# Kernel optimization log

Hardware: AMD Instinct MI355X
Metric: run time of the kernel (lower is better)

Reference implementation:

```python
import jax, jax.numpy as jnp
import numpy as np

B, S, HID = 1, 2048, 2048
H, KVH, D = 32, 8, 64
NUM_MASKS = 3
ROPE_THETA = 10000.0


def rope_tables(seq_len, dim, theta=ROPE_THETA):
    inv_freq = 1.0 / (theta ** (np.arange(0, dim, 2, dtype=np.float32) / dim))
    t = np.arange(seq_len, dtype=np.float32)
    freqs = np.outer(t, inv_freq)                      # [S, D/2]
    emb = np.concatenate([freqs, freqs], axis=-1)      # [S, D]
    return jnp.asarray(np.cos(emb))[None], jnp.asarray(np.sin(emb))[None]  # [1,S,D]


def setup_inputs() -> dict:
    key = jax.random.key(0)
    ks = jax.random.split(key, 5)
    cos, sin = rope_tables(S, D)
    sc = 1.0 / np.sqrt(HID)
    return {
        "hidden_states": jax.random.normal(ks[0], (B, S, HID), jnp.float32),
        "cos": cos, "sin": sin,
        "Wq": jax.random.normal(ks[1], (HID, H * D), jnp.float32) * sc,
        "Wk": jax.random.normal(ks[2], (HID, KVH * D), jnp.float32) * sc,
        "Wv": jax.random.normal(ks[3], (HID, KVH * D), jnp.float32) * sc,
        "Wo": jax.random.normal(ks[4], (H * D, HID), jnp.float32) * sc,
        "num_masks": NUM_MASKS,
    }


def rotate_half(x):
    x1, x2 = jnp.split(x, 2, axis=-1)
    return jnp.concatenate([-x2, x1], axis=-1)


def block_causal_bias(seq_len, num_mask, dtype):
    block_size = num_mask + 1
    i = jnp.arange(seq_len)[:, None]
    j = jnp.arange(seq_len)[None, :]
    causal = j <= i
    column = causal & (j % (num_mask + 1) == 0)
    block = causal & ((i // block_size) == (j // block_size))
    allowed = column | block
    neg = jnp.asarray(jnp.finfo(dtype).min if dtype != jnp.float32 else -jnp.inf, dtype)
    return jnp.where(allowed, jnp.asarray(0.0, dtype), neg)  # [S,S]


def reference(hidden_states, cos, sin, Wq, Wk, Wv, Wo, num_masks):
    b, s, _ = hidden_states.shape
    scaling = D ** -0.5
    # projections -> [B, heads, S, D]
    q = (hidden_states @ Wq).reshape(b, s, H, D).transpose(0, 2, 1, 3)
    k = (hidden_states @ Wk).reshape(b, s, KVH, D).transpose(0, 2, 1, 3)
    v = (hidden_states @ Wv).reshape(b, s, KVH, D).transpose(0, 2, 1, 3)
    # RoPE (cos/sin: [1,S,D] -> [1,1,S,D])
    c, sn = cos[:, None], sin[:, None]
    q = q * c + rotate_half(q) * sn
    k = k * c + rotate_half(k) * sn
    # GQA: repeat kv heads
    g = H // KVH
    k = jnp.repeat(k, g, axis=1)
    v = jnp.repeat(v, g, axis=1)
    bias = block_causal_bias(s, num_masks, hidden_states.dtype)  # [S,S]
    scores = jnp.einsum("bhqd,bhkd->bhqk", q, k) * scaling + bias[None, None]
    probs = jax.nn.softmax(scores, axis=-1)
    out = jnp.einsum("bhqk,bhkd->bhqd", probs, v)  # [B,H,S,D]
    out = out.transpose(0, 2, 1, 3).reshape(b, s, H * D)
    return out @ Wo
```

## Files before the change

### kernel.cpp

```cpp
#include <hip/hip_runtime.h>
#include <hip/hip_bf16.h>
#include <stdint.h>

#define S_LEN  2048
#define HIDDEN 2048
#define NH     32
#define NKVH   8
#define HD     64
#define NHD    (NH*HD)
#define KVD    (NKVH*HD)

typedef __attribute__((ext_vector_type(8))) short  short8;
typedef __attribute__((ext_vector_type(4))) short  short4v;
typedef __attribute__((ext_vector_type(4))) float  f32x4;
typedef __attribute__((ext_vector_type(4))) float  float4v;
typedef __attribute__((ext_vector_type(8))) __bf16 bf16x8;

#define WAITVM8()  asm volatile("s_waitcnt vmcnt(8)" ::: "memory")
#define WAITVM4()  asm volatile("s_waitcnt vmcnt(4)" ::: "memory")
#define WAITVM0()  asm volatile("s_waitcnt vmcnt(0)" ::: "memory")
#define ABARRIER() asm volatile("s_barrier" ::: "memory")

__device__ __forceinline__ short f2bf(float x){
  uint32_t u = __builtin_bit_cast(uint32_t, x);
  u += 0x7fffu + ((u >> 16) & 1u);
  return (short)(u >> 16);
}

__device__ __forceinline__ f32x4 mfma_bf16(short8 a, short8 b, f32x4 c){
  return __builtin_amdgcn_mfma_f32_16x16x32_bf16(
      __builtin_bit_cast(bf16x8, a), __builtin_bit_cast(bf16x8, b), c, 0, 0, 0);
}

__device__ __forceinline__ void gload16(const short* g, short* l){
  __builtin_amdgcn_global_load_lds(
      (const __attribute__((address_space(1))) void*)g,
      (__attribute__((address_space(3))) void*)l, 16, 0, 0);
}

__global__ __launch_bounds__(256) void k_prep(const float* __restrict__ hs,
                                              short* __restrict__ hsb,
                                              const float* __restrict__ Wq, short* __restrict__ WqT,
                                              const float* __restrict__ Wk, short* __restrict__ WkT,
                                              const float* __restrict__ Wv, short* __restrict__ WvT){
  int bid = blockIdx.x;
  if (bid < 4096){
    int i = bid*256 + threadIdx.x;
    float4v v = ((const float4v* __restrict__)hs)[i];
    short4v o;
#pragma unroll
    for (int j=0;j<4;j++) o[j] = f2bf(v[j]);
    ((short4v* __restrict__)hsb)[i] = o;
    return;
  }
  bid -= 4096;
  const float* W; short* WT; int R, C, GX;
  if (bid < 4096)      { W = Wq; WT = WqT; R = HIDDEN; C = NHD; GX = 64; }
  else if (bid < 5120) { bid -= 4096; W = Wk; WT = WkT; R = HIDDEN; C = KVD; GX = 16; }
  else                 { bid -= 5120; W = Wv; WT = WvT; R = HIDDEN; C = KVD; GX = 16; }
  const int bx = bid % GX, by = bid / GX;
  __shared__ float tile[32][33];
  const int x = threadIdx.x & 31, y0 = threadIdx.x >> 5;
  const int c0 = bx*32, r0 = by*32;
#pragma unroll
  for (int yy=y0; yy<32; yy+=8) tile[yy][x] = W[(size_t)(r0+yy)*C + c0 + x];
  __syncthreads();
#pragma unroll
  for (int yy=y0; yy<32; yy+=8) WT[(size_t)(c0+yy)*R + r0 + x] = f2bf(tile[x][yy]);
}

struct GemmIdx {
  int wid, r, g, wr, wc, kg, gtid, srow, c8, sx;
};
__device__ __forceinline__ GemmIdx gemm_idx(){
  GemmIdx ix;
  int tid = threadIdx.x, lane = tid&63;
  ix.kg = tid>>8; ix.gtid = tid&255;
  ix.wid = (tid>>6)&3; ix.r = lane&15; ix.g = lane>>4;
  ix.wr = ix.wid>>1; ix.wc = ix.wid&1;
  const int gt = ix.gtid;
  const int row0 = ((gt>>2) ^ (gt>>4)) & 1;
  ix.srow = (((gt>>3)<<1) | row0);
  ix.c8   = ((gt ^ (gt>>2) ^ (gt>>4)) & 1) | ((((gt>>1) ^ (gt>>3)) & 1) << 1);
  ix.sx   = (ix.r & 7) << 3;
  return ix;
}

__device__ __forceinline__ void compute128(const short* As, const short* Bs,
                                           f32x4 acc[4][4], const GemmIdx& ix){
  short8 af[4], bf[4];
#pragma unroll
  for (int m=0;m<4;m++)
    af[m] = *(const short8*)&As[((ix.wr*64 + m*16 + ix.r)*32 + ix.g*8) ^ ix.sx];
#pragma unroll
  for (int n=0;n<4;n++)
    bf[n] = *(const short8*)&Bs[((ix.wc*64 + n*16 + ix.r)*32 + ix.g*8) ^ ix.sx];
#pragma unroll
  for (int m=0;m<4;m++)
#pragma unroll
    for (int n=0;n<4;n++) acc[m][n] = mfma_bf16(af[m], bf[n], acc[m][n]);
}

__device__ __forceinline__ void red_groups(short* LDS, f32x4 acc[4][4], const GemmIdx& ix){
  __syncthreads();
  float* red = (float*)LDS;
  if (ix.kg){
#pragma unroll
    for (int m=0;m<4;m++)
#pragma unroll
      for (int n=0;n<4;n++)
#pragma unroll
        for (int j=0;j<4;j++)
          red[ix.wid*4096 + (m*16 + ix.g*4 + j)*64 + n*16 + ix.r] = acc[m][n][j];
  }
  __syncthreads();
  if (!ix.kg){
#pragma unroll
    for (int m=0;m<4;m++)
#pragma unroll
      for (int n=0;n<4;n++)
#pragma unroll
        for (int j=0;j<4;j++)
          acc[m][n][j] += red[ix.wid*4096 + (m*16 + ix.g*4 + j)*64 + n*16 + ix.r];
  }
}

template<int NKT>
__device__ __forceinline__ void gemm_core2(const short* __restrict__ A,
                                           const short* __restrict__ BT,
                                           int bm, int bn, short* LDS,
                                           f32x4 acc[4][4], const GemmIdx& ix){
  const int K = HIDDEN;
  const short* gA = A  + (size_t)(bm*128 + ix.srow)*K + ix.kg*(NKT*32) + ix.c8*8;
  const short* gB = BT + (size_t)(bn*128 + ix.srow)*K + ix.kg*(NKT*32) + ix.c8*8;
  short* L = LDS + ix.kg*16384;
  const int w = ix.gtid>>6;

#pragma unroll
  for (int m=0;m<4;m++)
#pragma unroll
    for (int n=0;n<4;n++) acc[m][n] = (f32x4){0.f,0.f,0.f,0.f};

  auto STAGE = [&](int buf, int kt){
    short* As_ = L + buf*8192;
    gload16(gA + kt*32,                As_ + w*512);
    gload16(gA + (size_t)64*K + kt*32, As_ + 2048 + w*512);
    gload16(gB + kt*32,                As_ + 4096 + w*512);
    gload16(gB + (size_t)64*K + kt*32, As_ + 6144 + w*512);
  };

  STAGE(0, 0);
  __syncthreads();
  for (int u=0; u<NKT/2; ++u){
    const int t = 2*u;
    if (t+1 < NKT) STAGE(1, t+1);
    compute128(L, L + 4096, acc, ix);
    __syncthreads();
    if (t+2 < NKT) STAGE(0, t+2);
    compute128(L + 8192, L + 12288, acc, ix);
    __syncthreads();
  }
  red_groups(LDS, acc, ix);
}

template<int NKT>
__device__ __forceinline__ void gemm_core3(const short* __restrict__ A,
                                           const short* __restrict__ BT,
                                           int bm, int bn, short* LDS,
                                           f32x4 acc[4][4], const GemmIdx& ix){
  const int K = HIDDEN;
  const short* gA = A  + (size_t)(bm*128 + ix.srow)*K + ix.kg*(NKT*32) + ix.c8*8;
  const short* gB = BT + (size_t)(bn*128 + ix.srow)*K + ix.kg*(NKT*32) + ix.c8*8;
  short* L = LDS + ix.kg*24576;
  const int w = ix.gtid>>6;

#pragma unroll
  for (int m=0;m<4;m++)
#pragma unroll
    for (int n=0;n<4;n++) acc[m][n] = (f32x4){0.f,0.f,0.f,0.f};

  auto STAGE = [&](int buf, int kt){
    short* As_ = L + buf*8192;
    gload16(gA + kt*32,                As_ + w*512);
    gload16(gA + (size_t)64*K + kt*32, As_ + 2048 + w*512);
    gload16(gB + kt*32,                As_ + 4096 + w*512);
    gload16(gB + (size_t)64*K + kt*32, As_ + 6144 + w*512);
  };

  STAGE(0, 0);
  STAGE(1, 1);
  int cur = 0;
  for (int t=0; t<NKT-2; ++t){
    int nxt = cur+2; if (nxt>=3) nxt-=3;
    STAGE(nxt, t+2);
    WAITVM8();
    ABARRIER();
    compute128(L + cur*8192, L + cur*8192 + 4096, acc, ix);
    ABARRIER();
    cur = (cur==2) ? 0 : cur+1;
  }
  WAITVM4();
  ABARRIER();
  compute128(L + cur*8192, L + cur*8192 + 4096, acc, ix);
  ABARRIER();
  cur = (cur==2) ? 0 : cur+1;
  WAITVM0();
  ABARRIER();
  compute128(L + cur*8192, L + cur*8192 + 4096, acc, ix);

  red_groups(LDS, acc, ix);
}

__global__ __launch_bounds__(512, 4) void k_gemm_qkv(const short* __restrict__ hsb,
                                                     const short* __restrict__ WqT,
                                                     const short* __restrict__ WkT,
                                                     const short* __restrict__ WvT,
                                                     const float* __restrict__ cosT,
                                                     const float* __restrict__ sinT,
                                                     const int* __restrict__ nm,
                                                     const float* __restrict__ Wo,
                                                     short* __restrict__ WoT,
                                                     short* __restrict__ Qb,
                                                     short* __restrict__ Kb,
                                                     short* __restrict__ VT,
                                                     short* __restrict__ VTs){
  __shared__ short LDS[32768];
  const int bn = blockIdx.x, bm = blockIdx.y;
  GemmIdx ix = gemm_idx();
  f32x4 acc[4][4];

  if (bn < 16){
    gemm_core2<32>(hsb, WqT + (size_t)bn*128*HIDDEN, bm, 0, LDS, acc, ix);
    if (ix.kg) return;
    const int h2 = bn*2 + ix.wc;
#pragma unroll
    for (int m=0;m<4;m++)
#pragma unroll
      for (int j=0;j<4;j++){
        const int s = bm*128 + ix.wr*64 + m*16 + ix.g*4 + j;
        const float* cr = cosT + s*64;
        const float* sr = sinT + s*64;
#pragma unroll
        for (int n=0;n<2;n++){
          const int d = n*16 + ix.r;
          float x1 = acc[m][n][j], x2 = acc[m][n+2][j];
          Qb[(size_t)s*NHD + h2*64 + d]      = f2bf((x1*cr[d]    - x2*sr[d])   *0.125f);
          Qb[(size_t)s*NHD + h2*64 + d + 32] = f2bf((x2*cr[d+32] + x1*sr[d+32])*0.125f);
        }
      }
  } else if (bn < 20){
    gemm_core2<32>(hsb, WkT + (size_t)(bn-16)*128*HIDDEN, bm, 0, LDS, acc, ix);
    if (ix.kg) return;
    const int h2 = (bn-16)*2 + ix.wc;
#pragma unroll
    for (int m=0;m<4;m++)
#pragma unroll
      for (int j=0;j<4;j++){
        const int s = bm*128 + ix.wr*64 + m*16 + ix.g*4 + j;
        const float* cr = cosT + s*64;
        const float* sr = sinT + s*64;
#pragma unroll
        for (int n=0;n<2;n++){
          const int d = n*16 + ix.r;
          float x1 = acc[m][n][j], x2 = acc[m][n+2][j];
          Kb[(size_t)s*KVD + h2*64 + d]      = f2bf(x1*cr[d]    - x2*sr[d]);
          Kb[(size_t)s*KVD + h2*64 + d + 32] = f2bf(x2*cr[d+32] + x1*sr[d+32]);
        }
      }
  } else if (bn < 24){
    gemm_core2<32>(hsb, WvT + (size_t)(bn-20)*128*HIDDEN, bm, 0, LDS, acc, ix);
    const int bs  = nm[0] + 1;
    const int lbs = 31 - __clz(bs);
    const int d0  = (bn-20)*128;
    const int s0  = bm*128;
    short* Vt = LDS;
    __syncthreads();
    if (!ix.kg){
#pragma unroll
      for (int n=0;n<4;n++){
        const int dr = ix.wc*64 + n*16 + ix.r;
#pragma unroll
        for (int m=0;m<4;m++){
          const int sc_ = ix.wr*64 + m*16 + ix.g*4;
          short4v o;
#pragma unroll
          for (int j=0;j<4;j++) o[j] = f2bf(acc[m][n][j]);
          *(short4v*)&Vt[dr*136 + sc_] = o;
        }
      }
    }
    __syncthreads();
    const int tid = threadIdx.x;
#pragma unroll
    for (int it=0; it<4; ++it){
      const int row = tid>>2, c8 = (tid&3)*32 + it*8;
      *(short8*)&VT[(size_t)(d0+row)*S_LEN + s0 + c8] = *(short8*)&Vt[row*136 + c8];
    }
    const int cnt = 128 >> lbs;
    for (int e = tid; e < 128*cnt; e += 512){
      const int row = e >> (7 - lbs), c = e & (cnt - 1);
      VTs[(size_t)(d0+row)*S_LEN + (s0>>lbs) + c] = Vt[row*136 + (c<<lbs)];
    }
  } else {
    const int bnt = bn - 24;
    float* tf = (float*)LDS;
    const int tid = threadIdx.x;
    const int half = tid >> 8;
    const int x = tid & 31, y0 = (tid >> 5) & 7;
    const int c0base = bnt*512, r0base = bm*128;
    for (int it=0; it<32; ++it){
      const int t = it*2 + half;
      const int c0 = c0base + (t & 15)*32;
      const int r0 = r0base + (t >> 4)*32;
      __syncthreads();
#pragma unroll
      for (int yy=y0; yy<32; yy+=8)
        tf[half*1056 + yy*33 + x] = Wo[(size_t)(r0+yy)*HIDDEN + c0 + x];
      __syncthreads();
#pragma unroll
      for (int yy=y0; yy<32; yy+=8)
        WoT[(size_t)(c0+yy)*NHD + r0 + x] = f2bf(tf[half*1056 + x*33 + yy]);
    }
  }
}

__global__ __launch_bounds__(512, 4) void k_gemm(const short* __restrict__ A,
                                                 const short* __restrict__ BT,
                                                 float* __restrict__ C, int Nc){
  __shared__ short LDS[49152];
  const int bn = blockIdx.x, bm = blockIdx.y;
  GemmIdx ix = gemm_idx();
  f32x4 acc[4][4];
  gemm_core3<32>(A, BT, bm, bn, LDS, acc, ix);
  if (ix.kg) return;
#pragma unroll
  for (int m=0;m<4;m++)
#pragma unroll
    for (int n=0;n<4;n++)
#pragma unroll
      for (int j=0;j<4;j++)
        C[(size_t)(bm*128 + ix.wr*64 + m*16 + ix.g*4 + j)*Nc
          + bn*128 + ix.wc*64 + n*16 + ix.r] = acc[m][n][j];
}


#define BF16_ONE 16256

__device__ __forceinline__ void sm_pv1(f32x4 sc[4],
                                       f32x4& accl,
                                       f32x4 acc[4], short* Pw,
                                       const short* Vtile,
                                       int r, int g){
  const short8 ones = {BF16_ONE,BF16_ONE,BF16_ONE,BF16_ONE,
                       BF16_ONE,BF16_ONE,BF16_ONE,BF16_ONE};
#pragma unroll
  for (int n=0;n<4;n++)
#pragma unroll
    for (int j=0;j<4;j++)
      Pw[(g*4+j)*72 + n*16 + r] = f2bf(__expf(sc[n][j]));

  short8 pf0 = *(short8*)&Pw[r*72 + g*8];
  short8 pf1 = *(short8*)&Pw[r*72 + 32 + g*8];
  accl = mfma_bf16(pf0, ones, accl);
  accl = mfma_bf16(pf1, ones, accl);
#pragma unroll
  for (int f=0;f<4;f++){
    short8 vf0 = *(const short8*)(Vtile + (size_t)(f*16 + r)*S_LEN + g*8);
    short8 vf1 = *(const short8*)(Vtile + (size_t)(f*16 + r)*S_LEN + 32 + g*8);
    acc[f] = mfma_bf16(pf0, vf0, acc[f]);
    acc[f] = mfma_bf16(pf1, vf1, acc[f]);
  }
}

__global__ __launch_bounds__(64, 4) void k_attn3(const short* __restrict__ Qb,
                                                 const short* __restrict__ Kb,
                                                 const short* __restrict__ VT,
                                                 const short* __restrict__ VTs,
                                                 const int* __restrict__ nm,
                                                 short* __restrict__ Ob){
  const int i  = gridDim.x - 1 - blockIdx.x;
  const int qs = i >> 5;
  const int h  = i & 31;
  const int hk = h >> 2;
  const int bs = nm[0] + 1;

  const int lane = threadIdx.x;
  const int r = lane&15, g = lane>>4;

  __shared__ short Pw[16*72];

  const int qlo = qs*16;

  short8 qf0 = *(const short8*)(Qb + (size_t)(qlo + r)*NHD + h*HD + g*8);
  short8 qf1 = *(const short8*)(Qb + (size_t)(qlo + r)*NHD + h*HD + 32 + g*8);

  f32x4 acc[4];
  f32x4 accl = (f32x4){0.f,0.f,0.f,0.f};
#pragma unroll
  for (int f=0;f<4;f++) acc[f] = (f32x4){0.f,0.f,0.f,0.f};

  const short* Kg  = Kb  + hk*HD;
  const short* Vsg = VTs + (size_t)hk*HD*S_LEN;
  const short* Vdg = VT  + (size_t)hk*HD*S_LEN;

  const int cmax = qlo / bs;
  const int nct = (cmax + 63) >> 6;
  for (int ct=0; ct<nct; ++ct){
    const int cbase = ct*64;
    f32x4 sc[4];
#pragma unroll
    for (int n=0;n<4;n++){
      const int key = bs*(cbase + n*16 + r);
      short8 kf0 = *(const short8*)(Kg + (size_t)key*KVD + g*8);
      short8 kf1 = *(const short8*)(Kg + (size_t)key*KVD + 32 + g*8);
      f32x4 z = (f32x4){0.f,0.f,0.f,0.f};
      z = mfma_bf16(qf0, kf0, z);
      sc[n] = mfma_bf16(qf1, kf1, z);
    }
    if (cmax - cbase < 64){
#pragma unroll
      for (int n=0;n<4;n++){
        if (cbase + n*16 + r >= cmax){
#pragma unroll
          for (int j=0;j<4;j++) sc[n][j] = -1e30f;
        }
      }
    }
    sm_pv1(sc, accl, acc, Pw, Vsg + cbase, r, g);
  }

  {
    const short8 ones = {BF16_ONE,BF16_ONE,BF16_ONE,BF16_ONE,
                         BF16_ONE,BF16_ONE,BF16_ONE,BF16_ONE};
    const int key = qlo + r;
    short8 kf0 = *(const short8*)(Kg + (size_t)key*KVD + g*8);
    short8 kf1 = *(const short8*)(Kg + (size_t)key*KVD + 32 + g*8);
    f32x4 z = (f32x4){0.f,0.f,0.f,0.f};
    z = mfma_bf16(qf0, kf0, z);
    f32x4 sc0 = mfma_bf16(qf1, kf1, z);

    const int rb = r / bs, rm = r % bs;
#pragma unroll
    for (int j=0;j<4;j++){
      const int qrel = g*4 + j;
      bool ok = (r <= qrel) && ((rm == 0) || (rb == qrel/bs));
      sc0[j] = ok ? sc0[j] : -1e30f;
    }

#pragma unroll
    for (int j=0;j<4;j++){
      Pw[(g*4+j)*72 + r]      = f2bf(__expf(sc0[j]));
      Pw[(g*4+j)*72 + 16 + r] = 0;
    }
    short8 pf0 = *(short8*)&Pw[r*72 + g*8];
    accl = mfma_bf16(pf0, ones, accl);
#pragma unroll
    for (int f=0;f<4;f++){
      short8 vf0 = *(const short8*)(Vdg + (size_t)(f*16 + r)*S_LEN + qlo + g*8);
      acc[f] = mfma_bf16(pf0, vf0, acc[f]);
    }
  }

#pragma unroll
  for (int j=0;j<4;j++){
    float inv = 1.f / accl[j];
    const int q = qlo + g*4 + j;
#pragma unroll
    for (int f=0;f<4;f++)
      Ob[(size_t)q*NHD + h*HD + f*16 + r] = f2bf(acc[f][j]*inv);
  }
}

extern "C" void kernel_launch(void* const* d_in, const int* in_sizes, int n_in,
                              void* d_out, int out_size, void* d_ws, size_t ws_size,
                              hipStream_t stream){
  const float* hs   = (const float*)d_in[0];
  const float* cosT = (const float*)d_in[1];
  const float* sinT = (const float*)d_in[2];
  const float* Wq   = (const float*)d_in[3];
  const float* Wk   = (const float*)d_in[4];
  const float* Wv   = (const float*)d_in[5];
  const float* Wo   = (const float*)d_in[6];
  const int*   nm   = (const int*)d_in[7];

  char* ws = (char*)d_ws;
  short* hsb  = (short*)(ws);
  short* WqT  = (short*)(ws + (8ull<<20));
  short* WkT  = (short*)(ws + (16ull<<20));
  short* WvT  = (short*)(ws + (18ull<<20));
  short* WoT  = (short*)(ws + (20ull<<20));
  short* Qb   = (short*)(ws + (28ull<<20));
  short* Kb   = (short*)(ws + (36ull<<20));
  short* VT   = (short*)(ws + (38ull<<20));
  short* VTs  = (short*)(ws + (40ull<<20));
  short* attnb= (short*)(ws + (42ull<<20));
  float* out  = (float*)d_out;

  k_prep<<<dim3(10240), 256, 0, stream>>>(hs, hsb, Wq, WqT, Wk, WkT, Wv, WvT);

  k_gemm_qkv<<<dim3(28, 16), 512, 0, stream>>>(hsb, WqT, WkT, WvT, cosT, sinT, nm,
                                               Wo, WoT, Qb, Kb, VT, VTs);

  k_attn3<<<dim3((S_LEN/16)*NH), 64, 0, stream>>>(Qb, Kb, VT, VTs, nm, attnb);

  k_gemm<<<dim3(NHD/128, S_LEN/128), 512, 0, stream>>>(attnb, WoT, out, HIDDEN);
}
```

Before: 122.3 us.

## Process 32 query rows per attention wave and prefetch next key tile

```diff
diff --git a/kernel.cpp b/kernel.cpp
--- a/kernel.cpp
+++ b/kernel.cpp
@@ -346,33 +346,42 @@
 
 #define BF16_ONE 16256
 
-__device__ __forceinline__ void sm_pv1(f32x4 sc[4],
-                                       f32x4& accl,
-                                       f32x4 acc[4], short* Pw,
+__device__ __forceinline__ void sm_pv2(f32x4 sc[2][4],
+                                       f32x4 accl[2],
+                                       f32x4 acc[2][4], short* Pw,
                                        const short* Vtile,
                                        int r, int g){
   const short8 ones = {BF16_ONE,BF16_ONE,BF16_ONE,BF16_ONE,
                        BF16_ONE,BF16_ONE,BF16_ONE,BF16_ONE};
 #pragma unroll
-  for (int n=0;n<4;n++)
-#pragma unroll
-    for (int j=0;j<4;j++)
-      Pw[(g*4+j)*72 + n*16 + r] = f2bf(__expf(sc[n][j]));
-
-  short8 pf0 = *(short8*)&Pw[r*72 + g*8];
-  short8 pf1 = *(short8*)&Pw[r*72 + 32 + g*8];
-  accl = mfma_bf16(pf0, ones, accl);
-  accl = mfma_bf16(pf1, ones, accl);
+  for (int m=0;m<2;m++)
+#pragma unroll
+    for (int n=0;n<4;n++)
+#pragma unroll
+      for (int j=0;j<4;j++)
+        Pw[(m*16 + g*4 + j)*72 + n*16 + r] = f2bf(__expf(sc[m][n][j]));
+
+  short8 pf[2][2];
+#pragma unroll
+  for (int m=0;m<2;m++){
+    pf[m][0] = *(short8*)&Pw[(m*16 + r)*72 + g*8];
+    pf[m][1] = *(short8*)&Pw[(m*16 + r)*72 + 32 + g*8];
+    accl[m] = mfma_bf16(pf[m][0], ones, accl[m]);
+    accl[m] = mfma_bf16(pf[m][1], ones, accl[m]);
+  }
 #pragma unroll
   for (int f=0;f<4;f++){
     short8 vf0 = *(const short8*)(Vtile + (size_t)(f*16 + r)*S_LEN + g*8);
     short8 vf1 = *(const short8*)(Vtile + (size_t)(f*16 + r)*S_LEN + 32 + g*8);
-    acc[f] = mfma_bf16(pf0, vf0, acc[f]);
-    acc[f] = mfma_bf16(pf1, vf1, acc[f]);
-  }
-}
-
-__global__ __launch_bounds__(64, 4) void k_attn3(const short* __restrict__ Qb,
+#pragma unroll
+    for (int m=0;m<2;m++){
+      acc[m][f] = mfma_bf16(pf[m][0], vf0, acc[m][f]);
+      acc[m][f] = mfma_bf16(pf[m][1], vf1, acc[m][f]);
+    }
+  }
+}
+
+__global__ __launch_bounds__(64, 3) void k_attn4(const short* __restrict__ Qb,
                                                  const short* __restrict__ Kb,
                                                  const short* __restrict__ VT,
                                                  const short* __restrict__ VTs,
@@ -387,17 +396,25 @@
   const int lane = threadIdx.x;
   const int r = lane&15, g = lane>>4;
 
-  __shared__ short Pw[16*72];
-
-  const int qlo = qs*16;
-
-  short8 qf0 = *(const short8*)(Qb + (size_t)(qlo + r)*NHD + h*HD + g*8);
-  short8 qf1 = *(const short8*)(Qb + (size_t)(qlo + r)*NHD + h*HD + 32 + g*8);
-
-  f32x4 acc[4];
-  f32x4 accl = (f32x4){0.f,0.f,0.f,0.f};
-#pragma unroll
-  for (int f=0;f<4;f++) acc[f] = (f32x4){0.f,0.f,0.f,0.f};
+  __shared__ short Pw[32*72];
+
+  const int qlo = qs*32;
+
+  short8 qf[2][2];
+#pragma unroll
+  for (int m=0;m<2;m++){
+    qf[m][0] = *(const short8*)(Qb + (size_t)(qlo + m*16 + r)*NHD + h*HD + g*8);
+    qf[m][1] = *(const short8*)(Qb + (size_t)(qlo + m*16 + r)*NHD + h*HD + 32 + g*8);
+  }
+
+  f32x4 acc[2][4];
+  f32x4 accl[2];
+#pragma unroll
+  for (int m=0;m<2;m++){
+    accl[m] = (f32x4){0.f,0.f,0.f,0.f};
+#pragma unroll
+    for (int f=0;f<4;f++) acc[m][f] = (f32x4){0.f,0.f,0.f,0.f};
+  }
 
   const short* Kg  = Kb  + hk*HD;
   const short* Vsg = VTs + (size_t)hk*HD*S_LEN;
@@ -405,70 +422,115 @@
 
   const int cmax = qlo / bs;
   const int nct = (cmax + 63) >> 6;
+
+  short8 kp[4][2];
+  auto LOADK = [&](int cbase){
+#pragma unroll
+    for (int n=0;n<4;n++){
+      const int key = bs*(cbase + n*16 + r);
+      kp[n][0] = *(const short8*)(Kg + (size_t)key*KVD + g*8);
+      kp[n][1] = *(const short8*)(Kg + (size_t)key*KVD + 32 + g*8);
+    }
+  };
+
+  if (nct > 0) LOADK(0);
   for (int ct=0; ct<nct; ++ct){
     const int cbase = ct*64;
-    f32x4 sc[4];
+    f32x4 sc[2][4];
 #pragma unroll
     for (int n=0;n<4;n++){
-      const int key = bs*(cbase + n*16 + r);
-      short8 kf0 = *(const short8*)(Kg + (size_t)key*KVD + g*8);
-      short8 kf1 = *(const short8*)(Kg + (size_t)key*KVD + 32 + g*8);
-      f32x4 z = (f32x4){0.f,0.f,0.f,0.f};
-      z = mfma_bf16(qf0, kf0, z);
-      sc[n] = mfma_bf16(qf1, kf1, z);
-    }
+      const short8 kf0 = kp[n][0], kf1 = kp[n][1];
+#pragma unroll
+      for (int m=0;m<2;m++){
+        f32x4 z = (f32x4){0.f,0.f,0.f,0.f};
+        z = mfma_bf16(qf[m][0], kf0, z);
+        sc[m][n] = mfma_bf16(qf[m][1], kf1, z);
+      }
+    }
+    if (ct+1 < nct) LOADK(cbase + 64);
     if (cmax - cbase < 64){
 #pragma unroll
       for (int n=0;n<4;n++){
         if (cbase + n*16 + r >= cmax){
 #pragma unroll
-          for (int j=0;j<4;j++) sc[n][j] = -1e30f;
+          for (int m=0;m<2;m++)
+#pragma unroll
+            for (int j=0;j<4;j++) sc[m][n][j] = -1e30f;
         }
       }
     }
-    sm_pv1(sc, accl, acc, Pw, Vsg + cbase, r, g);
+    sm_pv2(sc, accl, acc, Pw, Vsg + cbase, r, g);
   }
 
   {
     const short8 ones = {BF16_ONE,BF16_ONE,BF16_ONE,BF16_ONE,
                          BF16_ONE,BF16_ONE,BF16_ONE,BF16_ONE};
-    const int key = qlo + r;
-    short8 kf0 = *(const short8*)(Kg + (size_t)key*KVD + g*8);
-    short8 kf1 = *(const short8*)(Kg + (size_t)key*KVD + 32 + g*8);
-    f32x4 z = (f32x4){0.f,0.f,0.f,0.f};
-    z = mfma_bf16(qf0, kf0, z);
-    f32x4 sc0 = mfma_bf16(qf1, kf1, z);
-
-    const int rb = r / bs, rm = r % bs;
+    f32x4 sd[2][2];
+#pragma unroll
+    for (int n=0;n<2;n++){
+      const int key = qlo + n*16 + r;
+      short8 kf0 = *(const short8*)(Kg + (size_t)key*KVD + g*8);
+      short8 kf1 = *(const short8*)(Kg + (size_t)key*KVD + 32 + g*8);
+#pragma unroll
+      for (int m=0;m<2;m++){
+        f32x4 z = (f32x4){0.f,0.f,0.f,0.f};
+        z = mfma_bf16(qf[m][0], kf0, z);
+        sd[m][n] = mfma_bf16(qf[m][1], kf1, z);
+      }
+    }
+    int kdn[2]; bool kz[2];
+#pragma unroll
+    for (int n=0;n<2;n++){
+      const int krel = n*16 + r;
+      kdn[n] = krel / bs;
+      kz[n]  = (krel % bs) == 0;
+    }
+#pragma unroll
+    for (int m=0;m<2;m++)
+#pragma unroll
+      for (int j=0;j<4;j++){
+        const int qrel = m*16 + g*4 + j;
+        const int qd = qrel / bs;
+#pragma unroll
+        for (int n=0;n<2;n++){
+          const int krel = n*16 + r;
+          bool ok = (krel <= qrel) && (kz[n] || (kdn[n] == qd));
+          sd[m][n][j] = ok ? sd[m][n][j] : -1e30f;
+        }
+      }
+#pragma unroll
+    for (int m=0;m<2;m++)
+#pragma unroll
+      for (int n=0;n<2;n++)
+#pragma unroll
+        for (int j=0;j<4;j++)
+          Pw[(m*16 + g*4 + j)*72 + n*16 + r] = f2bf(__expf(sd[m][n][j]));
+
+    short8 pf[2];
+#pragma unroll
+    for (int m=0;m<2;m++){
+      pf[m] = *(short8*)&Pw[(m*16 + r)*72 + g*8];
+      accl[m] = mfma_bf16(pf[m], ones, accl[m]);
+    }
+#pragma unroll
+    for (int f=0;f<4;f++){
+      short8 vf = *(const short8*)(Vdg + (size_t)(f*16 + r)*S_LEN + qlo + g*8);
+#pragma unroll
+      for (int m=0;m<2;m++)
+        acc[m][f] = mfma_bf16(pf[m], vf, acc[m][f]);
+    }
+  }
+
+#pragma unroll
+  for (int m=0;m<2;m++)
 #pragma unroll
     for (int j=0;j<4;j++){
-      const int qrel = g*4 + j;
-      bool ok = (r <= qrel) && ((rm == 0) || (rb == qrel/bs));
-      sc0[j] = ok ? sc0[j] : -1e30f;
-    }
-
-#pragma unroll
-    for (int j=0;j<4;j++){
-      Pw[(g*4+j)*72 + r]      = f2bf(__expf(sc0[j]));
-      Pw[(g*4+j)*72 + 16 + r] = 0;
-    }
-    short8 pf0 = *(short8*)&Pw[r*72 + g*8];
-    accl = mfma_bf16(pf0, ones, accl);
-#pragma unroll
-    for (int f=0;f<4;f++){
-      short8 vf0 = *(const short8*)(Vdg + (size_t)(f*16 + r)*S_LEN + qlo + g*8);
-      acc[f] = mfma_bf16(pf0, vf0, acc[f]);
-    }
-  }
-
-#pragma unroll
-  for (int j=0;j<4;j++){
-    float inv = 1.f / accl[j];
-    const int q = qlo + g*4 + j;
-#pragma unroll
-    for (int f=0;f<4;f++)
-      Ob[(size_t)q*NHD + h*HD + f*16 + r] = f2bf(acc[f][j]*inv);
-  }
+      float inv = 1.f / accl[m][j];
+      const int q = qlo + m*16 + g*4 + j;
+#pragma unroll
+      for (int f=0;f<4;f++)
+        Ob[(size_t)q*NHD + h*HD + f*16 + r] = f2bf(acc[m][f][j]*inv);
+    }
 }
 
 extern "C" void kernel_launch(void* const* d_in, const int* in_sizes, int n_in,
@@ -501,7 +563,7 @@
   k_gemm_qkv<<<dim3(28, 16), 512, 0, stream>>>(hsb, WqT, WkT, WvT, cosT, sinT, nm,
                                                Wo, WoT, Qb, Kb, VT, VTs);
 
-  k_attn3<<<dim3((S_LEN/16)*NH), 64, 0, stream>>>(Qb, Kb, VT, VTs, nm, attnb);
+  k_attn4<<<dim3((S_LEN/32)*NH), 64, 0, stream>>>(Qb, Kb, VT, VTs, nm, attnb);
 
   k_gemm<<<dim3(NHD/128, S_LEN/128), 512, 0, stream>>>(attnb, WoT, out, HIDDEN);
 }
```

After: 109.2 us. -10.7%, faster.
